# Performance work log

Hardware: AMD Instinct MI355X
Metric: run time of the kernel (lower is better)

The kernel has to match this reference:

```python
import jax, jax.numpy as jnp
import numpy as np

BATCH, SEQ, IN_DIM, UNITS = 64, 2048, 256, 256


def _glorot(key, shape):
    lim = np.sqrt(6.0 / (shape[0] + shape[1]))
    return jax.random.uniform(key, shape, jnp.float32, -lim, lim)


def setup_inputs() -> dict:
    key = jax.random.key(0)
    ks = jax.random.split(key, 5)
    return {
        "inputs": jax.random.normal(ks[0], (BATCH, SEQ, IN_DIM), jnp.float32),
        "W_f": _glorot(ks[1], (IN_DIM, UNITS)),
        "U_f": _glorot(ks[2], (UNITS, UNITS)),
        "b_f": jnp.zeros((UNITS,), jnp.float32),
        "W_s": _glorot(ks[3], (IN_DIM, UNITS)),
        "U_s": _glorot(ks[4], (UNITS, UNITS)),
        "b_s": jnp.zeros((UNITS,), jnp.float32),
    }


def reference(inputs, W_f, U_f, b_f, W_s, U_s, b_s):
    # Precompute input projections for all timesteps (one big GEMM each).
    xf = jnp.einsum('bti,iu->btu', inputs, W_f) + b_f  # (B, T, U)
    xs = jnp.einsum('bti,iu->btu', inputs, W_s) + b_s  # (B, T, U)

    h0 = jnp.zeros((inputs.shape[0], U_f.shape[0]), inputs.dtype)

    def step(h, xt):
        xf_t, xs_t = xt
        f_t = jax.nn.sigmoid(xf_t + h @ U_f)
        s_tilde = jnp.tanh(xs_t + (f_t * h) @ U_s)
        h_new = (1.0 - f_t) * h + f_t * s_tilde
        return h_new, h_new

    # scan over time: move time axis to front
    _, hs = jax.lax.scan(step, h0, (jnp.swapaxes(xf, 0, 1), jnp.swapaxes(xs, 0, 1)))
    return jnp.swapaxes(hs, 0, 1)  # (B, T, U)
```

## Files before the change

kernel.cpp:

```cpp
#include <hip/hip_runtime.h>
#include <hip/hip_bf16.h>

#define BATCH 64
#define SEQ 2048
#define IN_DIM 256
#define UNITS 256

typedef _Float16 half2_t __attribute__((ext_vector_type(2)));

__device__ __forceinline__ float fdot2(half2_t a, half2_t b, float c) {
#if __has_builtin(__builtin_amdgcn_fdot2)
    return __builtin_amdgcn_fdot2(a, b, c, false);
#else
    return c + (float)a[0] * (float)b[0] + (float)a[1] * (float)b[1];
#endif
}

template <int CTRL>
__device__ __forceinline__ float dpp_xor_add(float v) {
    int s = __builtin_amdgcn_update_dpp(0, __float_as_int(v), CTRL, 0xF, 0xF, true);
    return v + __int_as_float(s);
}
__device__ __forceinline__ float row8_sum(float v) {
    v = dpp_xor_add<0xB1>(v);
    v = dpp_xor_add<0x4E>(v);
    v = dpp_xor_add<0x141>(v);
    return v;
}

#define BAR() asm volatile("s_waitcnt lgkmcnt(0)\n\ts_barrier" ::: "memory")

__global__ void prep_u(const float* __restrict__ Uf, const float* __restrict__ Us,
                       _Float16* __restrict__ Utf, _Float16* __restrict__ Uts) {
    int idx = blockIdx.x * 256 + threadIdx.x;
    int k = idx >> 8;
    int u = idx & 255;
    Utf[u * 256 + k] = (_Float16)Uf[idx];
    Uts[u * 256 + k] = (_Float16)Us[idx];
}

__global__ __launch_bounds__(256) void proj_kernel(
    const float* __restrict__ X,
    const float* __restrict__ Wf, const float* __restrict__ bf,
    const float* __restrict__ Wsm, const float* __restrict__ bs,
    float* __restrict__ xf_out, _Float16* __restrict__ xs_out)
{
    __shared__ float Xs[64][65];
    __shared__ float Wsh[64][68];

    const int tid = threadIdx.x;
    const int rt = blockIdx.x;
    const int ct = blockIdx.y;
    const int r0 = rt * 64;
    const bool is_f = ct < 4;
    const int c0 = (ct & 3) * 64;
    const float* W = is_f ? Wf : Wsm;
    const float* bias = is_f ? bf : bs;
    const int tx = tid & 15;
    const int ty = tid >> 4;

    float acc[4][4];
#pragma unroll
    for (int i = 0; i < 4; ++i)
#pragma unroll
        for (int j = 0; j < 4; ++j) acc[i][j] = 0.f;

    for (int kc = 0; kc < IN_DIM; kc += 64) {
        __syncthreads();
#pragma unroll
        for (int i = 0; i < 4; ++i) {
            int f = tid + i * 256;
            int row = f >> 4;
            int kq = f & 15;
            float4 v = *(const float4*)(X + (size_t)(r0 + row) * IN_DIM + kc + kq * 4);
            Xs[row][kq * 4 + 0] = v.x;
            Xs[row][kq * 4 + 1] = v.y;
            Xs[row][kq * 4 + 2] = v.z;
            Xs[row][kq * 4 + 3] = v.w;
        }
#pragma unroll
        for (int i = 0; i < 4; ++i) {
            int f = tid + i * 256;
            int kk = f >> 4;
            int n4 = f & 15;
            float4 v = *(const float4*)(W + (size_t)(kc + kk) * UNITS + c0 + n4 * 4);
            *(float4*)&Wsh[kk][n4 * 4] = v;
        }
        __syncthreads();
#pragma unroll 8
        for (int kk = 0; kk < 64; ++kk) {
            float a0 = Xs[tx * 4 + 0][kk];
            float a1 = Xs[tx * 4 + 1][kk];
            float a2 = Xs[tx * 4 + 2][kk];
            float a3 = Xs[tx * 4 + 3][kk];
            float4 bv = *(const float4*)&Wsh[kk][ty * 4];
            acc[0][0] += a0 * bv.x; acc[0][1] += a0 * bv.y; acc[0][2] += a0 * bv.z; acc[0][3] += a0 * bv.w;
            acc[1][0] += a1 * bv.x; acc[1][1] += a1 * bv.y; acc[1][2] += a1 * bv.z; acc[1][3] += a1 * bv.w;
            acc[2][0] += a2 * bv.x; acc[2][1] += a2 * bv.y; acc[2][2] += a2 * bv.z; acc[2][3] += a2 * bv.w;
            acc[3][0] += a3 * bv.x; acc[3][1] += a3 * bv.y; acc[3][2] += a3 * bv.z; acc[3][3] += a3 * bv.w;
        }
    }

#pragma unroll
    for (int i = 0; i < 4; ++i) {
        int r = r0 + tx * 4 + i;
        int n0 = c0 + ty * 4;
        if (is_f) {
            float4 v;
            v.x = acc[i][0] + bias[n0 + 0];
            v.y = acc[i][1] + bias[n0 + 1];
            v.z = acc[i][2] + bias[n0 + 2];
            v.w = acc[i][3] + bias[n0 + 3];
            *(float4*)(xf_out + (size_t)r * UNITS + n0) = v;
        } else {
#pragma unroll
            for (int j = 0; j < 4; ++j)
                xs_out[(size_t)r * UNITS + n0 + j] = (_Float16)(acc[i][j] + bias[n0 + j]);
        }
    }
}

__global__ __launch_bounds__(1024) void recur_kernel(
    float* xf_out,
    const _Float16* __restrict__ xs16,
    const _Float16* __restrict__ Utf,
    const _Float16* __restrict__ Uts)
{
    __shared__ __align__(16) _Float16 h2p[8 * 40];
    __shared__ __align__(16) _Float16 g2p[8 * 40];

    const int tid = threadIdx.x;
    const int w = tid >> 6;
    const int lane = tid & 63;
    const int g = lane & 7;
    const int r = lane >> 3;
    const int u0 = 16 * w + 2 * r;
    const int b = blockIdx.x;

    union F4H { float4 f4; half2_t h[4]; };
    union U2H { unsigned u; half2_t h; };

    half2_t uf[2][16], us[2][16];
#pragma unroll
    for (int i = 0; i < 2; ++i) {
        const float4* pf = (const float4*)(Utf + ((size_t)(u0 + i) * 256 + 32 * g));
        const float4* ps = (const float4*)(Uts + ((size_t)(u0 + i) * 256 + 32 * g));
#pragma unroll
        for (int jj = 0; jj < 4; ++jj) {
            F4H a; a.f4 = pf[jj];
            F4H c; c.f4 = ps[jj];
#pragma unroll
            for (int m = 0; m < 4; ++m) {
                uf[i][4 * jj + m] = a.h[m];
                us[i][4 * jj + m] = c.h[m];
            }
        }
    }

    if (tid < 8 * 40) h2p[tid] = (_Float16)0.f;

    const size_t base = (size_t)b * SEQ * UNITS;
    const int widx = (w >> 1) * 40 + 16 * (w & 1) + 2 * r;

    float h_old0 = 0.f, h_old1 = 0.f, f0 = 0.f, f1 = 0.f;
    float2 xf_cur = make_float2(0.f, 0.f);
    unsigned xs_cur = 0;
    if (g == 0) {
        xf_cur = *(const float2*)(xf_out + base + u0);
        xs_cur = *(const unsigned*)(xs16 + base + u0);
    }
    __syncthreads();

    for (int t = 0; t < SEQ; ++t) {
        const int tn = (t + 1 < SEQ) ? t + 1 : t;

        float2 xf_nxt = make_float2(0.f, 0.f);
        unsigned xs_nxt = 0;
        if (g == 0) {
            xf_nxt = *(const float2*)(xf_out + base + (size_t)tn * UNITS + u0);
            xs_nxt = *(const unsigned*)(xs16 + base + (size_t)tn * UNITS + u0);
        }

        {
            const float4* hv = (const float4*)(h2p + g * 40);
            F4H H0, H1, H2, H3;
            H0.f4 = hv[0]; H1.f4 = hv[1]; H2.f4 = hv[2]; H3.f4 = hv[3];
            float a0 = 0.f, a1 = 0.f;
#pragma unroll
            for (int m = 0; m < 4; ++m) {
                a0 = fdot2(uf[0][m +  0], H0.h[m], a0);
                a1 = fdot2(uf[1][m +  0], H0.h[m], a1);
                a0 = fdot2(uf[0][m +  4], H1.h[m], a0);
                a1 = fdot2(uf[1][m +  4], H1.h[m], a1);
                a0 = fdot2(uf[0][m +  8], H2.h[m], a0);
                a1 = fdot2(uf[1][m +  8], H2.h[m], a1);
                a0 = fdot2(uf[0][m + 12], H3.h[m], a0);
                a1 = fdot2(uf[1][m + 12], H3.h[m], a1);
            }
            a0 = row8_sum(a0);
            a1 = row8_sum(a1);
            if (g == 0) {
                f0 = 1.f / (1.f + __expf(-(xf_cur.x + a0)));
                f1 = 1.f / (1.f + __expf(-(xf_cur.y + a1)));
                half2_t gv;
                gv[0] = (_Float16)(f0 * h_old0);
                gv[1] = (_Float16)(f1 * h_old1);
                *(half2_t*)(g2p + widx) = gv;
            }
        }
        BAR();

        {
            const float4* gv4 = (const float4*)(g2p + g * 40);
            F4H G0, G1, G2, G3;
            G0.f4 = gv4[0]; G1.f4 = gv4[1]; G2.f4 = gv4[2]; G3.f4 = gv4[3];
            float c0 = 0.f, c1 = 0.f;
#pragma unroll
            for (int m = 0; m < 4; ++m) {
                c0 = fdot2(us[0][m +  0], G0.h[m], c0);
                c1 = fdot2(us[1][m +  0], G0.h[m], c1);
                c0 = fdot2(us[0][m +  4], G1.h[m], c0);
                c1 = fdot2(us[1][m +  4], G1.h[m], c1);
                c0 = fdot2(us[0][m +  8], G2.h[m], c0);
                c1 = fdot2(us[1][m +  8], G2.h[m], c1);
                c0 = fdot2(us[0][m + 12], G3.h[m], c0);
                c1 = fdot2(us[1][m + 12], G3.h[m], c1);
            }
            c0 = row8_sum(c0);
            c1 = row8_sum(c1);
            if (g == 0) {
                U2H xh; xh.u = xs_cur;
                float z0 = (float)xh.h[0] + c0;
                float z1 = (float)xh.h[1] + c1;
                z0 = fminf(fmaxf(z0, -15.f), 15.f);
                z1 = fminf(fmaxf(z1, -15.f), 15.f);
                float e0 = __expf(2.f * z0);
                float e1 = __expf(2.f * z1);
                float s0 = 1.f - 2.f / (e0 + 1.f);
                float s1 = 1.f - 2.f / (e1 + 1.f);
                float hn0 = h_old0 + f0 * (s0 - h_old0);
                float hn1 = h_old1 + f1 * (s1 - h_old1);
                h_old0 = hn0;
                h_old1 = hn1;
                half2_t hv2;
                hv2[0] = (_Float16)hn0;
                hv2[1] = (_Float16)hn1;
                *(half2_t*)(h2p + widx) = hv2;
                float2 st; st.x = hn0; st.y = hn1;
                *(float2*)(xf_out + base + (size_t)t * UNITS + u0) = st;
                xf_cur = xf_nxt;
                xs_cur = xs_nxt;
            }
        }
        BAR();
    }
}

extern "C" void kernel_launch(void* const* d_in, const int* in_sizes, int n_in,
                              void* d_out, int out_size, void* d_ws, size_t ws_size,
                              hipStream_t stream) {
    (void)in_sizes; (void)n_in; (void)out_size; (void)ws_size;

    const float* X   = (const float*)d_in[0];
    const float* Wf  = (const float*)d_in[1];
    const float* Uf  = (const float*)d_in[2];
    const float* bf  = (const float*)d_in[3];
    const float* Wsm = (const float*)d_in[4];
    const float* Us  = (const float*)d_in[5];
    const float* bs  = (const float*)d_in[6];
    float* out = (float*)d_out;

    _Float16* xs16 = (_Float16*)d_ws;
    _Float16* Utf  = xs16 + (size_t)BATCH * SEQ * UNITS;
    _Float16* Uts  = Utf + 256 * 256;

    prep_u<<<256, 256, 0, stream>>>(Uf, Us, Utf, Uts);
    proj_kernel<<<dim3(BATCH * SEQ / 64, 8), 256, 0, stream>>>(X, Wf, bf, Wsm, bs, out, xs16);
    recur_kernel<<<BATCH, 1024, 0, stream>>>(out, xs16, Utf, Uts);
}
```

Measured before the change: 4.266 ms.

## Halve recurrence block to 512 threads and spread gate epilogue across four lanes

The recurrence kernel now runs 8 waves instead of 16, with each 8-lane group computing four hidden units instead of two. The sigmoid/tanh epilogue now runs on four lanes per group (one unit each) instead of serially on lane 0. The aim is to shorten the two per-step barriers, which now span fewer waves, and the serial tail of each timestep. In exchange it doubles the register-resident U weights per thread and adds more dot-product work per lane. It also drops the tanh input clamp, relying on expf saturating to give ±1.

```diff
diff --git a/kernel.cpp b/kernel.cpp
--- a/kernel.cpp
+++ b/kernel.cpp
@@ -120,7 +120,7 @@
     }
 }
 
-__global__ __launch_bounds__(1024) void recur_kernel(
+__global__ __launch_bounds__(512) void recur_kernel(
     float* xf_out,
     const _Float16* __restrict__ xs16,
     const _Float16* __restrict__ Utf,
@@ -134,15 +134,14 @@
     const int lane = tid & 63;
     const int g = lane & 7;
     const int r = lane >> 3;
-    const int u0 = 16 * w + 2 * r;
+    const int u0 = 32 * w + 4 * r;
     const int b = blockIdx.x;
 
     union F4H { float4 f4; half2_t h[4]; };
-    union U2H { unsigned u; half2_t h; };
-
-    half2_t uf[2][16], us[2][16];
-#pragma unroll
-    for (int i = 0; i < 2; ++i) {
+
+    half2_t uf[4][16], us[4][16];
+#pragma unroll
+    for (int i = 0; i < 4; ++i) {
         const float4* pf = (const float4*)(Utf + ((size_t)(u0 + i) * 256 + 32 * g));
         const float4* ps = (const float4*)(Uts + ((size_t)(u0 + i) * 256 + 32 * g));
 #pragma unroll
@@ -160,94 +159,97 @@
     if (tid < 8 * 40) h2p[tid] = (_Float16)0.f;
 
     const size_t base = (size_t)b * SEQ * UNITS;
-    const int widx = (w >> 1) * 40 + 16 * (w & 1) + 2 * r;
-
-    float h_old0 = 0.f, h_old1 = 0.f, f0 = 0.f, f1 = 0.f;
-    float2 xf_cur = make_float2(0.f, 0.f);
-    unsigned xs_cur = 0;
-    if (g == 0) {
-        xf_cur = *(const float2*)(xf_out + base + u0);
-        xs_cur = *(const unsigned*)(xs16 + base + u0);
+
+    const bool wr = g < 4;
+    const int u = u0 + (g & 3);
+    const int lidx = w * 40 + 4 * r + (g & 3);
+
+    float h_old = 0.f;
+    float xf_cur = 0.f;
+    float xs_cur = 0.f;
+    if (wr) {
+        xf_cur = xf_out[base + u];
+        xs_cur = (float)xs16[base + u];
     }
     __syncthreads();
 
     for (int t = 0; t < SEQ; ++t) {
         const int tn = (t + 1 < SEQ) ? t + 1 : t;
 
-        float2 xf_nxt = make_float2(0.f, 0.f);
-        unsigned xs_nxt = 0;
-        if (g == 0) {
-            xf_nxt = *(const float2*)(xf_out + base + (size_t)tn * UNITS + u0);
-            xs_nxt = *(const unsigned*)(xs16 + base + (size_t)tn * UNITS + u0);
-        }
-
+        float xf_nxt = 0.f;
+        float xs_nxt = 0.f;
+        if (wr) {
+            xf_nxt = xf_out[base + (size_t)tn * UNITS + u];
+            xs_nxt = (float)xs16[base + (size_t)tn * UNITS + u];
+        }
+
+        float f;
         {
             const float4* hv = (const float4*)(h2p + g * 40);
             F4H H0, H1, H2, H3;
             H0.f4 = hv[0]; H1.f4 = hv[1]; H2.f4 = hv[2]; H3.f4 = hv[3];
-            float a0 = 0.f, a1 = 0.f;
+            float a0 = 0.f, a1 = 0.f, a2 = 0.f, a3 = 0.f;
 #pragma unroll
             for (int m = 0; m < 4; ++m) {
                 a0 = fdot2(uf[0][m +  0], H0.h[m], a0);
                 a1 = fdot2(uf[1][m +  0], H0.h[m], a1);
+                a2 = fdot2(uf[2][m +  0], H0.h[m], a2);
+                a3 = fdot2(uf[3][m +  0], H0.h[m], a3);
                 a0 = fdot2(uf[0][m +  4], H1.h[m], a0);
                 a1 = fdot2(uf[1][m +  4], H1.h[m], a1);
+                a2 = fdot2(uf[2][m +  4], H1.h[m], a2);
+                a3 = fdot2(uf[3][m +  4], H1.h[m], a3);
                 a0 = fdot2(uf[0][m +  8], H2.h[m], a0);
                 a1 = fdot2(uf[1][m +  8], H2.h[m], a1);
+                a2 = fdot2(uf[2][m +  8], H2.h[m], a2);
+                a3 = fdot2(uf[3][m +  8], H2.h[m], a3);
                 a0 = fdot2(uf[0][m + 12], H3.h[m], a0);
                 a1 = fdot2(uf[1][m + 12], H3.h[m], a1);
-            }
-            a0 = row8_sum(a0);
-            a1 = row8_sum(a1);
-            if (g == 0) {
-                f0 = 1.f / (1.f + __expf(-(xf_cur.x + a0)));
-                f1 = 1.f / (1.f + __expf(-(xf_cur.y + a1)));
-                half2_t gv;
-                gv[0] = (_Float16)(f0 * h_old0);
-                gv[1] = (_Float16)(f1 * h_old1);
-                *(half2_t*)(g2p + widx) = gv;
-            }
+                a2 = fdot2(uf[2][m + 12], H3.h[m], a2);
+                a3 = fdot2(uf[3][m + 12], H3.h[m], a3);
+            }
+            a0 = row8_sum(a0); a1 = row8_sum(a1);
+            a2 = row8_sum(a2); a3 = row8_sum(a3);
+            float av = (g == 0) ? a0 : (g == 1) ? a1 : (g == 2) ? a2 : a3;
+            f = 1.f / (1.f + __expf(-(xf_cur + av)));
+            if (wr) g2p[lidx] = (_Float16)(f * h_old);
         }
         BAR();
 
         {
-            const float4* gv4 = (const float4*)(g2p + g * 40);
+            const float4* gv = (const float4*)(g2p + g * 40);
             F4H G0, G1, G2, G3;
-            G0.f4 = gv4[0]; G1.f4 = gv4[1]; G2.f4 = gv4[2]; G3.f4 = gv4[3];
-            float c0 = 0.f, c1 = 0.f;
+            G0.f4 = gv[0]; G1.f4 = gv[1]; G2.f4 = gv[2]; G3.f4 = gv[3];
+            float c0 = 0.f, c1 = 0.f, c2 = 0.f, c3 = 0.f;
 #pragma unroll
             for (int m = 0; m < 4; ++m) {
                 c0 = fdot2(us[0][m +  0], G0.h[m], c0);
                 c1 = fdot2(us[1][m +  0], G0.h[m], c1);
+                c2 = fdot2(us[2][m +  0], G0.h[m], c2);
+                c3 = fdot2(us[3][m +  0], G0.h[m], c3);
                 c0 = fdot2(us[0][m +  4], G1.h[m], c0);
                 c1 = fdot2(us[1][m +  4], G1.h[m], c1);
+                c2 = fdot2(us[2][m +  4], G1.h[m], c2);
+                c3 = fdot2(us[3][m +  4], G1.h[m], c3);
                 c0 = fdot2(us[0][m +  8], G2.h[m], c0);
                 c1 = fdot2(us[1][m +  8], G2.h[m], c1);
+                c2 = fdot2(us[2][m +  8], G2.h[m], c2);
+                c3 = fdot2(us[3][m +  8], G2.h[m], c3);
                 c0 = fdot2(us[0][m + 12], G3.h[m], c0);
                 c1 = fdot2(us[1][m + 12], G3.h[m], c1);
-            }
-            c0 = row8_sum(c0);
-            c1 = row8_sum(c1);
-            if (g == 0) {
-                U2H xh; xh.u = xs_cur;
-                float z0 = (float)xh.h[0] + c0;
-                float z1 = (float)xh.h[1] + c1;
-                z0 = fminf(fmaxf(z0, -15.f), 15.f);
-                z1 = fminf(fmaxf(z1, -15.f), 15.f);
-                float e0 = __expf(2.f * z0);
-                float e1 = __expf(2.f * z1);
-                float s0 = 1.f - 2.f / (e0 + 1.f);
-                float s1 = 1.f - 2.f / (e1 + 1.f);
-                float hn0 = h_old0 + f0 * (s0 - h_old0);
-                float hn1 = h_old1 + f1 * (s1 - h_old1);
-                h_old0 = hn0;
-                h_old1 = hn1;
-                half2_t hv2;
-                hv2[0] = (_Float16)hn0;
-                hv2[1] = (_Float16)hn1;
-                *(half2_t*)(h2p + widx) = hv2;
-                float2 st; st.x = hn0; st.y = hn1;
-                *(float2*)(xf_out + base + (size_t)t * UNITS + u0) = st;
+                c2 = fdot2(us[2][m + 12], G3.h[m], c2);
+                c3 = fdot2(us[3][m + 12], G3.h[m], c3);
+            }
+            c0 = row8_sum(c0); c1 = row8_sum(c1);
+            c2 = row8_sum(c2); c3 = row8_sum(c3);
+            float cv = (g == 0) ? c0 : (g == 1) ? c1 : (g == 2) ? c2 : c3;
+            float e = __expf(2.f * (xs_cur + cv));
+            float s = 1.f - 2.f / (e + 1.f);
+            float hn = h_old + f * (s - h_old);
+            if (wr) {
+                h_old = hn;
+                h2p[lidx] = (_Float16)hn;
+                xf_out[base + (size_t)t * UNITS + u] = hn;
                 xf_cur = xf_nxt;
                 xs_cur = xs_nxt;
             }
@@ -276,5 +278,5 @@
 
     prep_u<<<256, 256, 0, stream>>>(Uf, Us, Utf, Uts);
     proj_kernel<<<dim3(BATCH * SEQ / 64, 8), 256, 0, stream>>>(X, Wf, bf, Wsm, bs, out, xs16);
-    recur_kernel<<<BATCH, 1024, 0, stream>>>(out, xs16, Utf, Uts);
-}
+    recur_kernel<<<BATCH, 512, 0, stream>>>(out, xs16, Utf, Uts);
+}
```

Result: faster. 3.614 ms (-15.3%).
